# Kernel tuning notes

Measured on AMD Instinct MI355X. Metric: run time of the kernel, lower is better.

Reference implementation:

```python
import jax, jax.numpy as jnp
import numpy as np
from jax import lax

IN_DIM, HID, OUT_DIM = 4, 20, 4
N = 2097152  # batch of collocation points
CHAIN_LENS = (16, 4, 1)


def swish(x):
    return x * jax.nn.sigmoid(x)


def _chain_params(key, length):
    ks = jax.random.split(key, 4)
    s = 0.1
    Wn = jax.random.normal(ks[0], (length, 3, HID, HID), jnp.float32) * s
    bn = jax.random.normal(ks[1], (length, 3, HID), jnp.float32) * s
    Wl = jax.random.normal(ks[2], (length, HID, HID), jnp.float32) * s
    bl = jax.random.normal(ks[3], (length, HID), jnp.float32) * s
    return Wn, bn, Wl, bl


def setup_inputs() -> dict:
    key = jax.random.key(0)
    ks = jax.random.split(key, 8)
    s = 0.1
    inp = {
        "x": jax.random.normal(ks[0], (N, IN_DIM), jnp.float32),
        "front_W": jax.random.normal(ks[1], (IN_DIM, HID), jnp.float32) * s,
        "front_b": jax.random.normal(ks[2], (HID,), jnp.float32) * s,
        "back_W": jax.random.normal(ks[3], (HID, OUT_DIM), jnp.float32) * s,
        "back_b": jax.random.normal(ks[4], (OUT_DIM,), jnp.float32) * s,
    }
    for i, L in enumerate(CHAIN_LENS):
        Wn, bn, Wl, bl = _chain_params(ks[5 + i], L)
        inp[f"Wn{i+1}"], inp[f"bn{i+1}"] = Wn, bn
        inp[f"Wl{i+1}"], inp[f"bl{i+1}"] = Wl, bl
    return inp


def _run_chain(h, Wn, bn, Wl, bl):
    # h: [N, HID]; Wn: [L,3,HID,HID]; bn: [L,3,HID]; Wl: [L,HID,HID]; bl: [L,HID]
    def body(h, p):
        Wn_i, bn_i, Wl_i, bl_i = p
        o = h
        for j in range(3):  # 3 Linear+Swish in block.net
            o = swish(o @ Wn_i[j] + bn_i[j])
        o2 = swish(h @ Wl_i + bl_i)  # block.lin shortcut
        return o + o2, None

    h, _ = lax.scan(body, h, (Wn, bn, Wl, bl))
    return h


def reference(x, front_W, front_b, back_W, back_b,
              Wn1, bn1, Wl1, bl1,
              Wn2, bn2, Wl2, bl2,
              Wn3, bn3, Wl3, bl3):
    h = x @ front_W + front_b  # [N, HID]
    x1 = _run_chain(h, Wn1, bn1, Wl1, bl1)
    x2 = _run_chain(h, Wn2, bn2, Wl2, bl2)
    x3 = _run_chain(h, Wn3, bn3, Wl3, bl3)
    return (x1 + x2 + x3) @ back_W + back_b  # [N, OUT_DIM]
```

## Files before the change

kernel.cpp:

```cpp
#include <hip/hip_runtime.h>
#include <stdint.h>

typedef uint32_t u32;
typedef uint16_t u16;
typedef _Float16 f16;
typedef __attribute__((ext_vector_type(2))) _Float16 h2;
typedef __attribute__((ext_vector_type(8))) _Float16 f16v8;
typedef __attribute__((ext_vector_type(16))) float f32x16;

#define N_MM 86
#define WS_NEED (N_MM * 2048)
#define LOG2E 1.44269504f

#define E0 0x37FE37FEu
#define E1 0xA909A909u
#define E2 0x19011901u
#define ONEF16 0x00003C00u

__device__ __forceinline__ u32 pkf16(float lo, float hi) {
  auto p = __builtin_amdgcn_cvt_pkrtz(lo, hi);
  return __builtin_bit_cast(u32, p);
}
__device__ __forceinline__ h2 uph(u32 v) { return __builtin_bit_cast(h2, v); }
__device__ __forceinline__ u32 phu(h2 v) { return __builtin_bit_cast(u32, v); }
__device__ __forceinline__ u32 pkadd(u32 a, u32 b) { return phu(uph(a) + uph(b)); }

__device__ __forceinline__ f16v8 as_f16(uint4 v) { return __builtin_bit_cast(f16v8, v); }

__device__ __forceinline__ f32x16 zero16() {
  f32x16 z = {0.f, 0.f, 0.f, 0.f, 0.f, 0.f, 0.f, 0.f,
              0.f, 0.f, 0.f, 0.f, 0.f, 0.f, 0.f, 0.f};
  return z;
}

__device__ __forceinline__ void swish5(const f32x16& t, uint4& o, u32& o4) {
  const h2 e0 = uph(E0), e1 = uph(E1), e2 = uph(E2);
  u32 r[5];
#pragma unroll
  for (int i = 0; i < 5; ++i) {
    h2 c = uph(pkf16(t[2 * i], t[2 * i + 1]));
    h2 s = c * c;
    h2 p = __builtin_elementwise_fma(e2, s, e1);
    p = __builtin_elementwise_fma(p, s, e0);
    r[i] = phu(__builtin_elementwise_fma(s, p, c));
  }
  o.x = r[0]; o.y = r[1]; o.z = r[2]; o.w = r[3]; o4 = r[4];
}

__device__ __forceinline__ f32x16 mm2b(uint4 a0, uint4 a1, uint4 b1, uint4 b2, const f32x16& Z) {
  f32x16 acc = __builtin_amdgcn_mfma_f32_32x32x16_f16(as_f16(a0), as_f16(b1), Z, 0, 0, 0);
  acc = __builtin_amdgcn_mfma_f32_32x32x16_f16(as_f16(a1), as_f16(b2), acc, 0, 0, 0);
  return acc;
}

__device__ __forceinline__ u16 f16bits(float v) {
  f16 h = (f16)v;
  return __builtin_bit_cast(u16, h);
}

__global__ void prep_kernel(
    const float* __restrict__ fW, const float* __restrict__ fb,
    const float* __restrict__ bW, const float* __restrict__ bb,
    const float* __restrict__ Wn1, const float* __restrict__ bn1,
    const float* __restrict__ Wl1, const float* __restrict__ bl1,
    const float* __restrict__ Wn2, const float* __restrict__ bn2,
    const float* __restrict__ Wl2, const float* __restrict__ bl2,
    const float* __restrict__ Wn3, const float* __restrict__ bn3,
    const float* __restrict__ Wl3, const float* __restrict__ bl3,
    u32* __restrict__ ws) {
  int mm = blockIdx.x;
  int lane = threadIdx.x;
  int m = lane & 31, g = lane >> 5;
  const float *W, *B;
  int M, Kmax, Mmax;
  float wscale, bscale;
  bool front = (mm == 0);
  if (mm == 0) { W = fW; B = fb; M = 20; Kmax = 4; Mmax = 20; wscale = 2.f; bscale = 2.f; }
  else if (mm == 85) { W = bW; B = bb; M = 4; Kmax = 20; Mmax = 4; wscale = 0.5f; bscale = 1.f; }
  else {
    int idx = mm - 1, bi = idx >> 2, j = idx & 3, lb;
    const float *Wn, *bn, *Wl, *bl;
    if (bi < 16)      { Wn = Wn1; bn = bn1; Wl = Wl1; bl = bl1; lb = bi; }
    else if (bi < 20) { Wn = Wn2; bn = bn2; Wl = Wl2; bl = bl2; lb = bi - 16; }
    else              { Wn = Wn3; bn = bn3; Wl = Wl3; bl = bl3; lb = 0; }
    if (j < 3) { W = Wn + (lb * 3 + j) * 400; B = bn + (lb * 3 + j) * 20; }
    else       { W = Wl + lb * 400;           B = bl + lb * 20; }
    M = 20; Kmax = 20; Mmax = 20; wscale = 0.5f; bscale = 1.f;
  }
  int ml = (m < 18) ? m : ((m >= 20 && m <= 21) ? m - 2 : -1);
  for (int f = 0; f < 2; ++f) {
    for (int r = 0; r < 4; ++r) {
      u32 v = 0;
      for (int hh = 0; hh < 2; ++hh) {
        int s = 2 * r + hh;
        int k = -1;
        bool bias = false;
        if (front) {
          if (f == 0 && g == 0) {
            if (s < 4) k = s;
            else if (s == 4) bias = true;
          }
        } else {
          if (f == 0) k = 4 * g + s + (s >= 4 ? 4 : 0);
          else if (g == 0) {
            if (s < 2) k = 16 + s;
            else if (s == 4) bias = true;
          } else {
            if (s < 2) k = 18 + s;
          }
        }
        u32 e = 0;
        if (ml >= 0 && ml < Mmax) {
          if (bias) e = f16bits(bscale * B[ml]);
          else if (k >= 0 && k < Kmax) e = f16bits(wscale * W[k * M + ml]);
        }
        v |= e << (16 * hh);
      }
      ws[mm * 512 + f * 256 + lane * 4 + r] = v;
    }
  }
}

__global__ __launch_bounds__(256) void reslinear_mfma(
    const float* __restrict__ x, const uint4* __restrict__ ws4,
    float* __restrict__ out, int ntiles2) {
  int lane = threadIdx.x & 63;
  int wave = threadIdx.x >> 6;
  int tile2 = blockIdx.x * 4 + wave;
  if (tile2 >= ntiles2) return;
  int n = lane & 31;
  bool hi = lane >= 32;
  int pt0 = tile2 * 64 + n;
  int pt1 = pt0 + 32;

  const f32x16 Z = zero16();
  const uint4* __restrict__ wlane = ws4 + lane;

  float4 x0 = ((const float4*)x)[pt0];
  float4 x1 = ((const float4*)x)[pt1];
  uint4 af = wlane[0];
  uint4 bfr0, bfr1;
  bfr0.x = pkf16(x0.x, x0.y); bfr0.y = pkf16(x0.z, x0.w); bfr0.z = ONEF16; bfr0.w = 0u;
  bfr1.x = pkf16(x1.x, x1.y); bfr1.y = pkf16(x1.z, x1.w); bfr1.z = ONEF16; bfr1.w = 0u;
  f32x16 t0 = __builtin_amdgcn_mfma_f32_32x32x16_f16(as_f16(af), as_f16(bfr0), Z, 0, 0, 0);
  f32x16 t1 = __builtin_amdgcn_mfma_f32_32x32x16_f16(as_f16(af), as_f16(bfr1), Z, 0, 0, 0);
  u32 h0[5], h1[5];
#pragma unroll
  for (int i = 0; i < 5; ++i) h0[i] = pkf16(t0[2 * i], t0[2 * i + 1]);
#pragma unroll
  for (int i = 0; i < 5; ++i) h1[i] = pkf16(t1[2 * i], t1[2 * i + 1]);

  u32 as0[5], as1[5];
#pragma unroll
  for (int i = 0; i < 5; ++i) { as0[i] = 0u; as1[i] = 0u; }

  uint4 cb1_0, cb2_0, ob1_0, ob2_0, pb1_0;
  uint4 cb1_1, cb2_1, ob1_1, ob2_1, pb1_1;
  u32 p4_0, p4_1;
  cb2_0.y = 0u; cb2_0.z = ONEF16; cb2_0.w = 0u;
  cb2_1.y = 0u; cb2_1.z = ONEF16; cb2_1.w = 0u;
  ob2_0.y = 0u; ob2_0.z = ONEF16; ob2_0.w = 0u;
  ob2_1.y = 0u; ob2_1.z = ONEF16; ob2_1.w = 0u;

  const int CH_L[3] = {16, 4, 1};
  const int CH_B[3] = {0, 16, 20};

  for (int c = 0; c < 3; ++c) {
    cb1_0.x = h0[0]; cb1_0.y = h0[1]; cb1_0.z = h0[2]; cb1_0.w = h0[3]; cb2_0.x = h0[4];
    cb1_1.x = h1[0]; cb1_1.y = h1[1]; cb1_1.z = h1[2]; cb1_1.w = h1[3]; cb2_1.x = h1[4];
    int L = CH_L[c];
    const uint4* __restrict__ wp = wlane + (size_t)(1 + CH_B[c] * 4) * 128;
    for (int b = 0; b < L; ++b) {
      uint4 a0, a1;

      a0 = wp[0]; a1 = wp[64]; wp += 128;
      t0 = mm2b(a0, a1, cb1_0, cb2_0, Z);
      t1 = mm2b(a0, a1, cb1_1, cb2_1, Z);
      swish5(t0, ob1_0, ob2_0.x); swish5(t1, ob1_1, ob2_1.x);

      a0 = wp[0]; a1 = wp[64]; wp += 128;
      t0 = mm2b(a0, a1, ob1_0, ob2_0, Z);
      t1 = mm2b(a0, a1, ob1_1, ob2_1, Z);
      swish5(t0, ob1_0, ob2_0.x); swish5(t1, ob1_1, ob2_1.x);

      a0 = wp[0]; a1 = wp[64]; wp += 128;
      t0 = mm2b(a0, a1, ob1_0, ob2_0, Z);
      t1 = mm2b(a0, a1, ob1_1, ob2_1, Z);
      swish5(t0, ob1_0, ob2_0.x); swish5(t1, ob1_1, ob2_1.x);

      a0 = wp[0]; a1 = wp[64]; wp += 128;
      t0 = mm2b(a0, a1, cb1_0, cb2_0, Z);
      t1 = mm2b(a0, a1, cb1_1, cb2_1, Z);
      swish5(t0, pb1_0, p4_0); swish5(t1, pb1_1, p4_1);

      cb1_0.x = pkadd(ob1_0.x, pb1_0.x);
      cb1_0.y = pkadd(ob1_0.y, pb1_0.y);
      cb1_0.z = pkadd(ob1_0.z, pb1_0.z);
      cb1_0.w = pkadd(ob1_0.w, pb1_0.w);
      cb2_0.x = pkadd(ob2_0.x, p4_0);
      cb1_1.x = pkadd(ob1_1.x, pb1_1.x);
      cb1_1.y = pkadd(ob1_1.y, pb1_1.y);
      cb1_1.z = pkadd(ob1_1.z, pb1_1.z);
      cb1_1.w = pkadd(ob1_1.w, pb1_1.w);
      cb2_1.x = pkadd(ob2_1.x, p4_1);
    }
    as0[0] = pkadd(as0[0], cb1_0.x);
    as0[1] = pkadd(as0[1], cb1_0.y);
    as0[2] = pkadd(as0[2], cb1_0.z);
    as0[3] = pkadd(as0[3], cb1_0.w);
    as0[4] = pkadd(as0[4], cb2_0.x);
    as1[0] = pkadd(as1[0], cb1_1.x);
    as1[1] = pkadd(as1[1], cb1_1.y);
    as1[2] = pkadd(as1[2], cb1_1.z);
    as1[3] = pkadd(as1[3], cb1_1.w);
    as1[4] = pkadd(as1[4], cb2_1.x);
  }

  {
    uint4 a0 = wlane[85 * 128];
    uint4 a1 = wlane[85 * 128 + 64];
    cb1_0.x = as0[0]; cb1_0.y = as0[1]; cb1_0.z = as0[2]; cb1_0.w = as0[3]; cb2_0.x = as0[4];
    cb1_1.x = as1[0]; cb1_1.y = as1[1]; cb1_1.z = as1[2]; cb1_1.w = as1[3]; cb2_1.x = as1[4];
    f32x16 r0 = mm2b(a0, a1, cb1_0, cb2_0, Z);
    f32x16 r1 = mm2b(a0, a1, cb1_1, cb2_1, Z);
    if (!hi) {
      ((float4*)out)[pt0] = make_float4(r0[0], r0[1], r0[2], r0[3]);
      ((float4*)out)[pt1] = make_float4(r1[0], r1[1], r1[2], r1[3]);
    }
  }
}

__device__ __forceinline__ float fast_exp2(float x) {
#if __has_builtin(__builtin_amdgcn_exp2f)
  return __builtin_amdgcn_exp2f(x);
#else
  return exp2f(x);
#endif
}
__device__ __forceinline__ float fast_rcp(float x) {
#if __has_builtin(__builtin_amdgcn_rcpf)
  return __builtin_amdgcn_rcpf(x);
#else
  return 1.0f / x;
#endif
}
__device__ __forceinline__ float swish_f(float x) {
  float e = fast_exp2(x * -LOG2E);
  return x * fast_rcp(1.0f + e);
}
__device__ __forceinline__ void matvec20f(float* __restrict__ t, const float* __restrict__ o,
                                          const float* __restrict__ W, const float* __restrict__ b) {
#pragma unroll
  for (int l = 0; l < 20; ++l) t[l] = b[l];
#pragma unroll
  for (int k = 0; k < 20; ++k) {
    float ok = o[k];
#pragma unroll
    for (int l = 0; l < 20; ++l) t[l] = fmaf(ok, W[k * 20 + l], t[l]);
  }
}
__global__ __launch_bounds__(256) void reslinear_fallback(
    const float* __restrict__ x, const float* __restrict__ fW, const float* __restrict__ fb,
    const float* __restrict__ bW, const float* __restrict__ bb,
    const float* __restrict__ Wn1, const float* __restrict__ bn1, const float* __restrict__ Wl1, const float* __restrict__ bl1,
    const float* __restrict__ Wn2, const float* __restrict__ bn2, const float* __restrict__ Wl2, const float* __restrict__ bl2,
    const float* __restrict__ Wn3, const float* __restrict__ bn3, const float* __restrict__ Wl3, const float* __restrict__ bl3,
    float* __restrict__ out, int np) {
  int tid = blockIdx.x * 256 + threadIdx.x;
  if (tid >= np) return;
  float4 d = ((const float4*)x)[tid];
  float xv[4] = {d.x, d.y, d.z, d.w};
  float h[20];
#pragma unroll
  for (int l = 0; l < 20; ++l) h[l] = fb[l];
#pragma unroll
  for (int k = 0; k < 4; ++k)
#pragma unroll
    for (int l = 0; l < 20; ++l) h[l] = fmaf(xv[k], fW[k * 20 + l], h[l]);
  float acc[20];
#pragma unroll
  for (int l = 0; l < 20; ++l) acc[l] = 0.f;
  for (int c = 0; c < 3; ++c) {
    const float* Wn = (c == 0) ? Wn1 : ((c == 1) ? Wn2 : Wn3);
    const float* bn = (c == 0) ? bn1 : ((c == 1) ? bn2 : bn3);
    const float* Wl = (c == 0) ? Wl1 : ((c == 1) ? Wl2 : Wl3);
    const float* bl = (c == 0) ? bl1 : ((c == 1) ? bl2 : bl3);
    const int L = (c == 0) ? 16 : ((c == 1) ? 4 : 1);
    float hc[20];
#pragma unroll
    for (int l = 0; l < 20; ++l) hc[l] = h[l];
    for (int i = 0; i < L; ++i) {
      float o[20], t[20];
#pragma unroll
      for (int l = 0; l < 20; ++l) o[l] = hc[l];
      for (int j = 0; j < 3; ++j) {
        matvec20f(t, o, Wn + j * 400, bn + j * 20);
#pragma unroll
        for (int l = 0; l < 20; ++l) o[l] = swish_f(t[l]);
      }
      matvec20f(t, hc, Wl, bl);
#pragma unroll
      for (int l = 0; l < 20; ++l) hc[l] = o[l] + swish_f(t[l]);
      Wn += 1200; bn += 60; Wl += 400; bl += 20;
    }
#pragma unroll
    for (int l = 0; l < 20; ++l) acc[l] += hc[l];
  }
  float r[4];
#pragma unroll
  for (int j = 0; j < 4; ++j) r[j] = bb[j];
#pragma unroll
  for (int k = 0; k < 20; ++k)
#pragma unroll
    for (int j = 0; j < 4; ++j) r[j] = fmaf(acc[k], bW[k * 4 + j], r[j]);
  ((float4*)out)[tid] = make_float4(r[0], r[1], r[2], r[3]);
}

extern "C" void kernel_launch(void* const* d_in, const int* in_sizes, int n_in,
                              void* d_out, int out_size, void* d_ws, size_t ws_size,
                              hipStream_t stream) {
  int np = in_sizes[0] / 4;

  if (ws_size >= (size_t)WS_NEED && (np % 64) == 0) {
    prep_kernel<<<N_MM, 64, 0, stream>>>(
        (const float*)d_in[1], (const float*)d_in[2], (const float*)d_in[3], (const float*)d_in[4],
        (const float*)d_in[5], (const float*)d_in[6], (const float*)d_in[7], (const float*)d_in[8],
        (const float*)d_in[9], (const float*)d_in[10], (const float*)d_in[11], (const float*)d_in[12],
        (const float*)d_in[13], (const float*)d_in[14], (const float*)d_in[15], (const float*)d_in[16],
        (u32*)d_ws);
    int ntiles2 = np / 64;
    int blocks = (ntiles2 + 3) / 4;
    reslinear_mfma<<<blocks, 256, 0, stream>>>(
        (const float*)d_in[0], (const uint4*)d_ws, (float*)d_out, ntiles2);
  } else {
    reslinear_fallback<<<(np + 255) / 256, 256, 0, stream>>>(
        (const float*)d_in[0], (const float*)d_in[1], (const float*)d_in[2], (const float*)d_in[3],
        (const float*)d_in[4], (const float*)d_in[5], (const float*)d_in[6], (const float*)d_in[7],
        (const float*)d_in[8], (const float*)d_in[9], (const float*)d_in[10], (const float*)d_in[11],
        (const float*)d_in[12], (const float*)d_in[13], (const float*)d_in[14], (const float*)d_in[15],
        (const float*)d_in[16], (float*)d_out, np);
  }
}
```

Baseline: 528.0 us.

## Reorder block matmuls to issue shortcut early and software-prefetch weights two stages ahead

```diff
diff --git a/kernel.cpp b/kernel.cpp
--- a/kernel.cpp
+++ b/kernel.cpp
@@ -78,7 +78,9 @@
   if (mm == 0) { W = fW; B = fb; M = 20; Kmax = 4; Mmax = 20; wscale = 2.f; bscale = 2.f; }
   else if (mm == 85) { W = bW; B = bb; M = 4; Kmax = 20; Mmax = 4; wscale = 0.5f; bscale = 1.f; }
   else {
-    int idx = mm - 1, bi = idx >> 2, j = idx & 3, lb;
+    int idx = mm - 1, bi = idx >> 2, p = idx & 3, lb;
+    const int jmap[4] = {0, 3, 1, 2};
+    int j = jmap[p];
     const float *Wn, *bn, *Wl, *bl;
     if (bi < 16)      { Wn = Wn1; bn = bn1; Wl = Wl1; bl = bl1; lb = bi; }
     else if (bi < 20) { Wn = Wn2; bn = bn2; Wl = Wl2; bl = bl2; lb = bi - 16; }
@@ -121,6 +123,41 @@
   }
 }
 
+
+#define ROT_PF()  { uint4 nl0 = pf[0], nl1 = pf[64]; pf += 128; \
+                    w0 = ca0; w1 = ca1; ca0 = na0; ca1 = na1; na0 = nl0; na1 = nl1; }
+#define ROT_NOPF() { w0 = ca0; w1 = ca1; ca0 = na0; ca1 = na1; }
+
+#define BLOCK_BODY(S3ROT)                                                    \
+  {                                                                          \
+    ROT_PF();                                        \
+    f32x16 t0 = mm2b(w0, w1, cb1_0, cb2_0, Z);                               \
+    f32x16 t1 = mm2b(w0, w1, cb1_1, cb2_1, Z);                               \
+    ROT_PF();         \
+    f32x16 u0 = mm2b(w0, w1, cb1_0, cb2_0, Z);                               \
+    f32x16 u1 = mm2b(w0, w1, cb1_1, cb2_1, Z);                               \
+    swish5(t0, ob1_0, ob2_0.x); swish5(t1, ob1_1, ob2_1.x);                  \
+    swish5(u0, pb1_0, p4_0);    swish5(u1, pb1_1, p4_1);                     \
+    ROT_PF();                                                     \
+    t0 = mm2b(w0, w1, ob1_0, ob2_0, Z);                                      \
+    t1 = mm2b(w0, w1, ob1_1, ob2_1, Z);                                      \
+    swish5(t0, ob1_0, ob2_0.x); swish5(t1, ob1_1, ob2_1.x);                  \
+    S3ROT();                                                      \
+    t0 = mm2b(w0, w1, ob1_0, ob2_0, Z);                                      \
+    t1 = mm2b(w0, w1, ob1_1, ob2_1, Z);                                      \
+    swish5(t0, ob1_0, ob2_0.x); swish5(t1, ob1_1, ob2_1.x);                  \
+    cb1_0.x = pkadd(ob1_0.x, pb1_0.x);                                       \
+    cb1_0.y = pkadd(ob1_0.y, pb1_0.y);                                       \
+    cb1_0.z = pkadd(ob1_0.z, pb1_0.z);                                       \
+    cb1_0.w = pkadd(ob1_0.w, pb1_0.w);                                       \
+    cb2_0.x = pkadd(ob2_0.x, p4_0);                                          \
+    cb1_1.x = pkadd(ob1_1.x, pb1_1.x);                                       \
+    cb1_1.y = pkadd(ob1_1.y, pb1_1.y);                                       \
+    cb1_1.z = pkadd(ob1_1.z, pb1_1.z);                                       \
+    cb1_1.w = pkadd(ob1_1.w, pb1_1.w);                                       \
+    cb2_1.x = pkadd(ob2_1.x, p4_1);                                          \
+  }
+
 __global__ __launch_bounds__(256) void reslinear_mfma(
     const float* __restrict__ x, const uint4* __restrict__ ws4,
     float* __restrict__ out, int ntiles2) {
@@ -136,9 +173,14 @@
   const f32x16 Z = zero16();
   const uint4* __restrict__ wlane = ws4 + lane;
 
+  uint4 af  = wlane[0];
+  uint4 ca0 = wlane[128], ca1 = wlane[192];
+  uint4 na0 = wlane[256], na1 = wlane[320];
+  const uint4* __restrict__ pf = wlane + 384;
+  uint4 w0, w1;
+
   float4 x0 = ((const float4*)x)[pt0];
   float4 x1 = ((const float4*)x)[pt1];
-  uint4 af = wlane[0];
   uint4 bfr0, bfr1;
   bfr0.x = pkf16(x0.x, x0.y); bfr0.y = pkf16(x0.z, x0.w); bfr0.z = ONEF16; bfr0.w = 0u;
   bfr1.x = pkf16(x1.x, x1.y); bfr1.y = pkf16(x1.z, x1.w); bfr1.z = ONEF16; bfr1.w = 0u;
@@ -162,47 +204,14 @@
   ob2_0.y = 0u; ob2_0.z = ONEF16; ob2_0.w = 0u;
   ob2_1.y = 0u; ob2_1.z = ONEF16; ob2_1.w = 0u;
 
-  const int CH_L[3] = {16, 4, 1};
-  const int CH_B[3] = {0, 16, 20};
-
-  for (int c = 0; c < 3; ++c) {
+  const int CH_L2[2] = {16, 4};
+
+  for (int c = 0; c < 2; ++c) {
     cb1_0.x = h0[0]; cb1_0.y = h0[1]; cb1_0.z = h0[2]; cb1_0.w = h0[3]; cb2_0.x = h0[4];
     cb1_1.x = h1[0]; cb1_1.y = h1[1]; cb1_1.z = h1[2]; cb1_1.w = h1[3]; cb2_1.x = h1[4];
-    int L = CH_L[c];
-    const uint4* __restrict__ wp = wlane + (size_t)(1 + CH_B[c] * 4) * 128;
+    int L = CH_L2[c];
     for (int b = 0; b < L; ++b) {
-      uint4 a0, a1;
-
-      a0 = wp[0]; a1 = wp[64]; wp += 128;
-      t0 = mm2b(a0, a1, cb1_0, cb2_0, Z);
-      t1 = mm2b(a0, a1, cb1_1, cb2_1, Z);
-      swish5(t0, ob1_0, ob2_0.x); swish5(t1, ob1_1, ob2_1.x);
-
-      a0 = wp[0]; a1 = wp[64]; wp += 128;
-      t0 = mm2b(a0, a1, ob1_0, ob2_0, Z);
-      t1 = mm2b(a0, a1, ob1_1, ob2_1, Z);
-      swish5(t0, ob1_0, ob2_0.x); swish5(t1, ob1_1, ob2_1.x);
-
-      a0 = wp[0]; a1 = wp[64]; wp += 128;
-      t0 = mm2b(a0, a1, ob1_0, ob2_0, Z);
-      t1 = mm2b(a0, a1, ob1_1, ob2_1, Z);
-      swish5(t0, ob1_0, ob2_0.x); swish5(t1, ob1_1, ob2_1.x);
-
-      a0 = wp[0]; a1 = wp[64]; wp += 128;
-      t0 = mm2b(a0, a1, cb1_0, cb2_0, Z);
-      t1 = mm2b(a0, a1, cb1_1, cb2_1, Z);
-      swish5(t0, pb1_0, p4_0); swish5(t1, pb1_1, p4_1);
-
-      cb1_0.x = pkadd(ob1_0.x, pb1_0.x);
-      cb1_0.y = pkadd(ob1_0.y, pb1_0.y);
-      cb1_0.z = pkadd(ob1_0.z, pb1_0.z);
-      cb1_0.w = pkadd(ob1_0.w, pb1_0.w);
-      cb2_0.x = pkadd(ob2_0.x, p4_0);
-      cb1_1.x = pkadd(ob1_1.x, pb1_1.x);
-      cb1_1.y = pkadd(ob1_1.y, pb1_1.y);
-      cb1_1.z = pkadd(ob1_1.z, pb1_1.z);
-      cb1_1.w = pkadd(ob1_1.w, pb1_1.w);
-      cb2_1.x = pkadd(ob2_1.x, p4_1);
+      BLOCK_BODY(ROT_PF)
     }
     as0[0] = pkadd(as0[0], cb1_0.x);
     as0[1] = pkadd(as0[1], cb1_0.y);
@@ -217,12 +226,26 @@
   }
 
   {
-    uint4 a0 = wlane[85 * 128];
-    uint4 a1 = wlane[85 * 128 + 64];
+    cb1_0.x = h0[0]; cb1_0.y = h0[1]; cb1_0.z = h0[2]; cb1_0.w = h0[3]; cb2_0.x = h0[4];
+    cb1_1.x = h1[0]; cb1_1.y = h1[1]; cb1_1.z = h1[2]; cb1_1.w = h1[3]; cb2_1.x = h1[4];
+    BLOCK_BODY(ROT_NOPF)
+    as0[0] = pkadd(as0[0], cb1_0.x);
+    as0[1] = pkadd(as0[1], cb1_0.y);
+    as0[2] = pkadd(as0[2], cb1_0.z);
+    as0[3] = pkadd(as0[3], cb1_0.w);
+    as0[4] = pkadd(as0[4], cb2_0.x);
+    as1[0] = pkadd(as1[0], cb1_1.x);
+    as1[1] = pkadd(as1[1], cb1_1.y);
+    as1[2] = pkadd(as1[2], cb1_1.z);
+    as1[3] = pkadd(as1[3], cb1_1.w);
+    as1[4] = pkadd(as1[4], cb2_1.x);
+  }
+
+  {
     cb1_0.x = as0[0]; cb1_0.y = as0[1]; cb1_0.z = as0[2]; cb1_0.w = as0[3]; cb2_0.x = as0[4];
     cb1_1.x = as1[0]; cb1_1.y = as1[1]; cb1_1.z = as1[2]; cb1_1.w = as1[3]; cb2_1.x = as1[4];
-    f32x16 r0 = mm2b(a0, a1, cb1_0, cb2_0, Z);
-    f32x16 r1 = mm2b(a0, a1, cb1_1, cb2_1, Z);
+    f32x16 r0 = mm2b(ca0, ca1, cb1_0, cb2_0, Z);
+    f32x16 r1 = mm2b(ca0, ca1, cb1_1, cb2_1, Z);
     if (!hi) {
       ((float4*)out)[pt0] = make_float4(r0[0], r0[1], r0[2], r0[3]);
       ((float4*)out)[pt1] = make_float4(r1[0], r1[1], r1[2], r1[3]);
```

Result: no change. 533.6 us (+1.1%).
